# Optimization experiments

Measured on AMD Instinct MI355X. Metric: run time of the kernel, lower is better.

The kernel has to match this reference:

```python
import jax, jax.numpy as jnp
import numpy as np

BN_EPS = 1e-5

def _bn_train(x, g, b):
    # BatchNorm1d in training mode: biased batch stats over the row dim
    m = x.mean(0)
    v = x.var(0)
    return g * (x - m) * jax.lax.rsqrt(v + BN_EPS) + b


def setup_inputs() -> dict:
    key = jax.random.key(0)
    ks = jax.random.split(key, 16)
    N, V, C, H, T, NC, OD, EH, EC = 128, 128, 256, 512, 12, 5, 5, 256, 256
    s = 0.05
    idx = jax.random.randint(ks[1], (T, N), 0, NC)
    return {
        "x": jax.random.normal(ks[0], (N, V, C), jnp.float32),
        "hidden_states": jnp.zeros((N, V, H), jnp.float32),
        "cell_states": jnp.zeros((N, V, H), jnp.float32),
        "one_hots_c_pred_seq": jax.nn.one_hot(idx, NC, dtype=jnp.float32),
        "W_ih": jax.random.normal(ks[2], (4 * H, C), jnp.float32) * s,
        "W_hh": jax.random.normal(ks[3], (4 * H, H), jnp.float32) * s,
        "b_ih": jax.random.normal(ks[4], (4 * H,), jnp.float32) * s,
        "b_hh": jax.random.normal(ks[5], (4 * H,), jnp.float32) * s,
        "W_cls": jax.random.normal(ks[6], (NC, H), jnp.float32) * s,
        "b_cls": jax.random.normal(ks[7], (NC,), jnp.float32) * s,
        "W_eh": jax.random.normal(ks[8], (EH, H), jnp.float32) * s,
        "b_eh": jax.random.normal(ks[9], (EH,), jnp.float32) * s,
        "g_eh": jnp.ones((EH,), jnp.float32),
        "beta_eh": jnp.zeros((EH,), jnp.float32),
        "W_ec": jax.random.normal(ks[10], (EC, NC), jnp.float32) * s,
        "b_ec": jax.random.normal(ks[11], (EC,), jnp.float32) * s,
        "g_ec": jnp.ones((EC,), jnp.float32),
        "beta_ec": jnp.zeros((EC,), jnp.float32),
        "W_out": jax.random.normal(ks[12], (OD, EH + EC), jnp.float32) * s,
        "b_out": jax.random.normal(ks[13], (OD,), jnp.float32) * s,
    }


def reference(x, hidden_states, cell_states, one_hots_c_pred_seq,
              W_ih, W_hh, b_ih, b_hh, W_cls, b_cls,
              W_eh, b_eh, g_eh, beta_eh, W_ec, b_ec, g_ec, beta_ec,
              W_out, b_out):
    N, V, C = x.shape
    H = hidden_states.shape[-1]
    xf = x.reshape(N * V, C)
    gx = xf @ W_ih.T + b_ih  # input gates are identical every step (x is repeated)

    def step(carry, onehot):
        h, c = carry  # [N*V, H]
        gates = gx + h @ W_hh.T + b_hh
        i, f, g, o = jnp.split(gates, 4, axis=1)  # pytorch LSTMCell gate order
        c = jax.nn.sigmoid(f) * c + jax.nn.sigmoid(i) * jnp.tanh(g)
        h = jax.nn.sigmoid(o) * jnp.tanh(c)
        # ClassifierLayer: avg-pool over V then 1x1 conv == mean + linear
        oc = h.reshape(N, V, H).mean(1) @ W_cls.T + b_cls  # [N, nc]
        # PredictionLayer
        eh = jax.nn.relu(_bn_train(h @ W_eh.T + b_eh, g_eh, beta_eh))
        ohr = jnp.broadcast_to(onehot[:, None, :], (N, V, onehot.shape[-1])).reshape(N * V, -1)
        ec = jax.nn.relu(_bn_train(ohr @ W_ec.T + b_ec, g_ec, beta_ec))
        op = jnp.concatenate([eh, ec], axis=1) @ W_out.T + b_out  # [N*V, out_dim]
        return (h, c), (op.reshape(N, V, -1), oc)

    carry0 = (hidden_states.reshape(N * V, H), cell_states.reshape(N * V, H))
    _, (preds, c_outs) = jax.lax.scan(step, carry0, one_hots_c_pred_seq)
    preds = preds.transpose(1, 0, 2, 3)  # [N, T, V, out_dim]
    # output_activation: bivariate-Gaussian params
    pred_outs = jnp.stack([preds[..., 0], preds[..., 1],
                           jnp.exp(preds[..., 2]), jnp.exp(preds[..., 3]),
                           jnp.tanh(preds[..., 4])], axis=-1)
    return pred_outs, c_outs
```

## Files before the change

kernel.cpp:

```cpp
#include <hip/hip_runtime.h>
#include <hip/hip_bf16.h>
#include <stdint.h>

typedef __hip_bfloat16 bf16;
typedef __attribute__((ext_vector_type(8))) short bf16x8;
typedef __attribute__((ext_vector_type(4))) short bf16x4;
typedef __attribute__((ext_vector_type(4))) float f32x4;

#define NN 128
#define VV 128
#define CC 256
#define HH 512
#define TT 12
#define NCLS 5
#define OD 5
#define EHD 256
#define KCAT (HH + CC)
#define ROWS (NN * VV)
#define PRED_SZ (NN * TT * VV * OD)
#define LDP 72
#define MiB (1ull << 20)


__device__ __forceinline__ float sigm(float x) {
    return __builtin_amdgcn_rcpf(1.f + __expf(-x));
}
__device__ __forceinline__ float tanh_(float x) {
    x = fminf(fmaxf(x, -15.f), 15.f);
    float e = __expf(2.f * x);
    return (e - 1.f) * __builtin_amdgcn_rcpf(e + 1.f);
}
__device__ __forceinline__ float bf2f(unsigned short v) {
    unsigned u = ((unsigned)v) << 16; float f; __builtin_memcpy(&f, &u, 4); return f;
}
__device__ __forceinline__ float ldin(const void* p, int i, int is32) {
    return is32 ? ((const float*)p)[i] : __bfloat162float(((const bf16*)p)[i]);
}

__device__ __forceinline__ void gl_lds16(const bf16* g, bf16* l) {
    __builtin_amdgcn_global_load_lds(
        (const __attribute__((address_space(1))) unsigned int*)g,
        (__attribute__((address_space(3))) unsigned int*)l, 16, 0, 0);
}


__device__ __forceinline__ void stage_t128s(const bf16* __restrict__ g, int ldg, int row0, int k0,
                                            bf16* lds) {
    int lane = threadIdx.x & 63, wave = threadIdx.x >> 6;
#pragma unroll
    for (int j = 0; j < 2; ++j) {
        int slot = j * 256 + wave * 64 + lane;
        int lds_row = slot >> 3;
        int bx = ((slot & 7) * 16) ^ ((lds_row & 7) << 4);
        int r = lds_row + 64 * (bx >> 6);
        int cb = bx & 63;
        gl_lds16(g + (size_t)(row0 + r) * ldg + k0 + (cb >> 1), lds + slot * 8);
    }
}
__device__ __forceinline__ void stage_t64s(const bf16* __restrict__ g, int ldg, int row0, int k0,
                                           bf16* lds) {
    int lane = threadIdx.x & 63, wave = threadIdx.x >> 6;
    int slot = wave * 64 + lane;
    int lds_row = slot >> 3;
    int bx = ((slot & 7) * 16) ^ ((lds_row & 7) << 4);
    int r = lds_row + 32 * (bx >> 6);
    int cb = bx & 63;
    gl_lds16(g + (size_t)(row0 + r) * ldg + k0 + (cb >> 1), lds + slot * 8);
}
__device__ __forceinline__ bf16x8 swz_rd(const bf16* base, int lds_row, int half, int eb) {
    int off = lds_row * 128 + ((half * 64 + eb) ^ ((lds_row & 7) << 4));
    return *(const bf16x8*)((const char*)base + off);
}
__device__ __forceinline__ void mfma_step32(const bf16* As, const bf16* Bs, f32x4 acc[4][4]) {
    const int lane = threadIdx.x & 63, wave = threadIdx.x >> 6;
    const int ha = wave >> 1, hb = wave & 1;
    const int l15 = lane & 15, eb = (lane >> 4) * 16;
    bf16x8 af[4], bg[4];
#pragma unroll
    for (int x = 0; x < 4; ++x) {
        af[x] = swz_rd(As, x * 16 + l15, ha, eb);
        bg[x] = swz_rd(Bs, x * 16 + l15, hb, eb);
    }
#pragma unroll
    for (int bi = 0; bi < 4; ++bi)
#pragma unroll
        for (int bj = 0; bj < 4; ++bj)
            acc[bi][bj] = __builtin_amdgcn_mfma_f32_16x16x32_bf16(af[bi], bg[bj], acc[bi][bj], 0, 0, 0);
}

__device__ __forceinline__ void stage128(const bf16* __restrict__ A, int lda, int row0,
                                         const bf16* __restrict__ B, int ldb, int col0,
                                         int k, bf16* As, bf16* Bs) {
    int lane = threadIdx.x & 63, wave = threadIdx.x >> 6;
    const bf16* pA = A + (size_t)(row0 + wave * 32 + (lane >> 3)) * lda + k + (lane & 7) * 8;
    const bf16* pB = B + (size_t)(col0 + wave * 32 + (lane >> 3)) * ldb + k + (lane & 7) * 8;
    bf16* lA = As + wave * 2048 + lane * 8;
    bf16* lB = Bs + wave * 2048 + lane * 8;
#pragma unroll
    for (int j = 0; j < 4; ++j) {
        gl_lds16(pA + (size_t)(j * 8) * lda, lA + j * 512);
        gl_lds16(pB + (size_t)(j * 8) * ldb, lB + j * 512);
    }
}
__device__ __forceinline__ void tile_mfma64(const bf16* As, const bf16* Bs, f32x4 acc[4][4]) {
    const int lane = threadIdx.x & 63, wave = threadIdx.x >> 6;
    const int wro = (wave >> 1) * 64, wco = (wave & 1) * 64;
    const int l15 = lane & 15, l8 = (lane >> 4) * 8;
#pragma unroll
    for (int kk = 0; kk < 64; kk += 32) {
        bf16x8 af[4], bg[4];
#pragma unroll
        for (int x = 0; x < 4; ++x) {
            af[x] = *(const bf16x8*)(As + (wro + x * 16 + l15) * 64 + kk + l8);
            bg[x] = *(const bf16x8*)(Bs + (wco + x * 16 + l15) * 64 + kk + l8);
        }
#pragma unroll
        for (int bi = 0; bi < 4; ++bi)
#pragma unroll
            for (int bj = 0; bj < 4; ++bj)
                acc[bi][bj] = __builtin_amdgcn_mfma_f32_16x16x32_bf16(af[bi], bg[bj], acc[bi][bj], 0, 0, 0);
    }
}

__global__ void detect_dtype(const void* g_eh, int* flag, int* hnz) {
    unsigned w = *(const unsigned*)g_eh;
    *flag = (w == 0x3F800000u) ? 1 : 0;
    *hnz = 0;
}

__global__ __launch_bounds__(256) void convert_in(const void* src, bf16* dst, int n, const int* flag) {
    int is32 = *flag;
    int i = blockIdx.x * 256 + threadIdx.x;
    int stride = gridDim.x * 256;
    if (is32) { const float* s = (const float*)src; for (; i < n; i += stride) dst[i] = __float2bfloat16(s[i]); }
    else      { const bf16*  s = (const bf16*)src;  for (; i < n; i += stride) dst[i] = s[i]; }
}

__global__ __launch_bounds__(256) void convert_in_hflag(const void* src, bf16* dst, int n, const int* flag,
                                                        int* nz) {
    int is32 = *flag;
    int i = blockIdx.x * 256 + threadIdx.x;
    int stride = gridDim.x * 256;
    int loc = 0;
    if (is32) {
        const float* s = (const float*)src;
        for (; i < n; i += stride) { float v = s[i]; if (__float_as_uint(v) != 0u) loc = 1; dst[i] = __float2bfloat16(v); }
    } else {
        const bf16* s = (const bf16*)src;
        for (; i < n; i += stride) { bf16 v = s[i]; if (*(const unsigned short*)&v) loc = 1; dst[i] = v; }
    }
    if (loc) atomicOr(nz, 1);
}

__global__ __launch_bounds__(256) void init_c(const void* cell, bf16* c, const int* flag) {
    int is32 = *flag;
    size_t i = (size_t)blockIdx.x * 256 + threadIdx.x;
    const size_t total = (size_t)ROWS * HH;
    for (; i < total; i += (size_t)8192 * 256) c[i] = __float2bfloat16(ldin(cell, (int)i, is32));
}

__device__ __forceinline__ void issue_loads(const bf16* __restrict__ A, int lda, int row0, int ka,
                                            const bf16* __restrict__ B, int ldb, int col0, int kb,
                                            bf16x8 ar[4], bf16x8 br[4]) {
    int tid = threadIdx.x;
#pragma unroll
    for (int it = 0; it < 4; ++it) {
        int cidx = tid + 256 * it;
        int row = cidx >> 3;
        int cc8 = (cidx & 7) * 8;
        ar[it] = *(const bf16x8*)(A + (size_t)(row0 + row) * lda + ka + cc8);
        br[it] = *(const bf16x8*)(B + (size_t)(col0 + row) * ldb + kb + cc8);
    }
}
__device__ __forceinline__ void write_lds(bf16* As, bf16* Bs, const bf16x8 ar[4], const bf16x8 br[4]) {
    int tid = threadIdx.x;
#pragma unroll
    for (int it = 0; it < 4; ++it) {
        int cidx = tid + 256 * it;
        int row = cidx >> 3;
        int cc8 = (cidx & 7) * 8;
        *(bf16x8*)(As + row * LDP + cc8) = ar[it];
        *(bf16x8*)(Bs + row * LDP + cc8) = br[it];
    }
}
__device__ __forceinline__ void tile_mfma(const bf16* As, const bf16* Bs, f32x4 acc[4][4]) {
    const int lane = threadIdx.x & 63, wave = threadIdx.x >> 6;
    const int wro = (wave >> 1) * 64, wco = (wave & 1) * 64;
    const int l15 = lane & 15, l8 = (lane >> 4) * 8;
#pragma unroll
    for (int kk = 0; kk < 64; kk += 32) {
        bf16x8 af[4], bg[4];
#pragma unroll
        for (int x = 0; x < 4; ++x) {
            af[x] = *(const bf16x8*)(As + (wro + x * 16 + l15) * LDP + kk + l8);
            bg[x] = *(const bf16x8*)(Bs + (wco + x * 16 + l15) * LDP + kk + l8);
        }
#pragma unroll
        for (int bi = 0; bi < 4; ++bi)
#pragma unroll
            for (int bj = 0; bj < 4; ++bj)
                acc[bi][bj] = __builtin_amdgcn_mfma_f32_16x16x32_bf16(af[bi], bg[bj], acc[bi][bj], 0, 0, 0);
    }
}

__global__ __launch_bounds__(256) void prep_weights(const void* __restrict__ Wih, const void* __restrict__ Whh,
                                                    const void* __restrict__ bih, const void* __restrict__ bhh,
                                                    bf16* __restrict__ Wihp, bf16* __restrict__ Whhp,
                                                    float* __restrict__ biasp, const int* flag) {
    int is32 = *flag;
    int jg = blockIdx.x;
    int b = jg >> 7, j = jg & 127;
    int gate = (j >> 4) & 3;
    int unit = b * 32 + (j & 15) + 16 * (j >> 6);
    int p = gate * HH + unit;
    for (int k = threadIdx.x; k < HH; k += 256)
        Whhp[(size_t)jg * HH + k] = __float2bfloat16(ldin(Whh, p * HH + k, is32));
    for (int k = threadIdx.x; k < CC; k += 256)
        Wihp[(size_t)jg * CC + k] = __float2bfloat16(ldin(Wih, p * CC + k, is32));
    if (threadIdx.x == 0)
        biasp[jg] = ldin(bih, p, is32) + ldin(bhh, p, is32);
}

__global__ __launch_bounds__(256) void gemm_k0(const bf16* __restrict__ A, const bf16* __restrict__ B,
                                               const float* __restrict__ biasp, bf16* __restrict__ gx) {
    __shared__ bf16 As[128 * 64], Bs[128 * 64];
    f32x4 acc[4][4] = {};
    int row0 = blockIdx.x * 128, col0 = blockIdx.y * 128;
    for (int k0 = 0; k0 < CC; k0 += 64) {
        __syncthreads();
        stage128(A, CC, row0, B, CC, col0, k0, As, Bs);
        __syncthreads();
        tile_mfma64(As, Bs, acc);
    }
    int lane = threadIdx.x & 63, wave = threadIdx.x >> 6;
    int wro = (wave >> 1) * 64, wco = (wave & 1) * 64;
    int l15 = lane & 15, lr4 = (lane >> 4) * 4;
#pragma unroll
    for (int bj = 0; bj < 4; ++bj) {
        int j = wco + bj * 16 + l15;
        float bia = biasp[col0 + j];
        int sidx = wco + l15 * 4 + bj;
#pragma unroll
        for (int bi = 0; bi < 4; ++bi)
#pragma unroll
            for (int reg = 0; reg < 4; ++reg) {
                int r = row0 + wro + bi * 16 + lr4 + reg;
                gx[(size_t)r * 2048 + col0 + sidx] = __float2bfloat16(acc[bi][bj][reg] + bia);
            }
    }
}

__global__ __launch_bounds__(256) void ec_precompute(const void* __restrict__ W_ec, const void* __restrict__ b_ec,
                                                     const void* __restrict__ g_ec, const void* __restrict__ beta_ec,
                                                     const void* __restrict__ W_out, const void* __restrict__ b_out,
                                                     const void* __restrict__ onehot, float* __restrict__ ecd_all,
                                                     const int* flag) {
    __shared__ float ecv[NCLS][EHD];
    __shared__ float cntf[NCLS];
    __shared__ float ecdc[NCLS][OD];
    int is32 = *flag;
    int t = blockIdx.x, tid = threadIdx.x;
    int ohoff = t * NN * NCLS;
    if (tid < NCLS) {
        float cnum = 0.f;
        for (int n = 0; n < NN; ++n) cnum += ldin(onehot, ohoff + n * NCLS + tid, is32);
        cntf[tid] = cnum * (1.f / NN);
    }
    __syncthreads();
    {
        int j = tid;
        float vals[NCLS];
        float m = 0.f, e2 = 0.f;
        float be = ldin(b_ec, j, is32);
        for (int cc = 0; cc < NCLS; ++cc) {
            vals[cc] = ldin(W_ec, j * NCLS + cc, is32) + be;
            m += cntf[cc] * vals[cc];
            e2 += cntf[cc] * vals[cc] * vals[cc];
        }
        float rs = rsqrtf(e2 - m * m + 1e-5f);
        float g = ldin(g_ec, j, is32), bt = ldin(beta_ec, j, is32);
        for (int cc = 0; cc < NCLS; ++cc)
            ecv[cc][j] = fmaxf(g * (vals[cc] - m) * rs + bt, 0.f);
    }
    __syncthreads();
    if (tid < NCLS * OD) {
        int cc = tid / OD, k = tid % OD;
        float s = 0.f;
        for (int j = 0; j < EHD; ++j) s += ecv[cc][j] * ldin(W_out, k * (EHD * 2) + EHD + j, is32);
        ecdc[cc][k] = s;
    }
    __syncthreads();
    if (tid < NN) {
        for (int k = 0; k < OD; ++k) {
            float s = ldin(b_out, k, is32);
            for (int cc = 0; cc < NCLS; ++cc) s += ldin(onehot, ohoff + tid * NCLS + cc, is32) * ecdc[cc][k];
            ecd_all[((size_t)t * NN + tid) * OD + k] = s;
        }
    }
}

__device__ __forceinline__ void final_rows(int grp, const bf16* __restrict__ ehp, const float* __restrict__ colsum,
                                           const float* __restrict__ colss, const void* __restrict__ g_eh,
                                           const void* __restrict__ beta_eh, const float* __restrict__ ecd_all,
                                           const float* Wl, void* __restrict__ out, int t, int is32) {
    int wave = threadIdx.x >> 6, lane = threadIdx.x & 63;
    int r = grp * 4 + wave;
    int j0 = lane * 4;
    float av[4], bv[4];
#pragma unroll
    for (int e = 0; e < 4; ++e) {
        float mean = colsum[j0 + e] * (1.f / ROWS);
        float var = colss[j0 + e] * (1.f / ROWS) - mean * mean;
        float a = ldin(g_eh, j0 + e, is32) * rsqrtf(var + 1e-5f);
        av[e] = a;
        bv[e] = ldin(beta_eh, j0 + e, is32) - mean * a;
    }
    bf16x4 xs = *(const bf16x4*)(ehp + (size_t)r * EHD + j0);
    float v0 = fmaxf(av[0] * bf2f((unsigned short)xs[0]) + bv[0], 0.f);
    float v1 = fmaxf(av[1] * bf2f((unsigned short)xs[1]) + bv[1], 0.f);
    float v2 = fmaxf(av[2] * bf2f((unsigned short)xs[2]) + bv[2], 0.f);
    float v3 = fmaxf(av[3] * bf2f((unsigned short)xs[3]) + bv[3], 0.f);
    float p[OD];
#pragma unroll
    for (int k = 0; k < OD; ++k)
        p[k] = v0 * Wl[k * EHD + j0] + v1 * Wl[k * EHD + j0 + 1] + v2 * Wl[k * EHD + j0 + 2] + v3 * Wl[k * EHD + j0 + 3];
#pragma unroll
    for (int off = 32; off; off >>= 1)
#pragma unroll
        for (int k = 0; k < OD; ++k) p[k] += __shfl_down(p[k], off, 64);
    if (lane == 0) {
        int n = r >> 7, v = r & 127;
        const float* en = ecd_all + ((size_t)t * NN + n) * OD;
        float o0 = p[0] + en[0];
        float o1 = p[1] + en[1];
        float o2 = expf(p[2] + en[2]);
        float o3 = expf(p[3] + en[3]);
        float o4 = tanh_(p[4] + en[4]);
        size_t base = (size_t)n * (TT * VV * OD) + (size_t)t * (VV * OD) + (size_t)v * OD;
        if (is32) {
            float* dst = (float*)out + base;
            dst[0] = o0; dst[1] = o1; dst[2] = o2; dst[3] = o3; dst[4] = o4;
        } else {
            bf16* dst = (bf16*)out + base;
            dst[0] = __float2bfloat16(o0);
            dst[1] = __float2bfloat16(o1);
            dst[2] = __float2bfloat16(o2);
            dst[3] = __float2bfloat16(o3);
            dst[4] = __float2bfloat16(o4);
        }
    }
}

__global__ __launch_bounds__(256) void lstm_fused(const bf16* __restrict__ h_in, const bf16* __restrict__ Whhp,
                                                  const bf16* __restrict__ gx, bf16* __restrict__ c,
                                                  bf16* __restrict__ h_out, float* __restrict__ csum_cur,
                                                  float* __restrict__ colsum_z, float* __restrict__ colss_z,
                                                  const bf16* __restrict__ Weh, const void* __restrict__ b_eh,
                                                  bf16* __restrict__ ehp_w, float* __restrict__ colsum_w,
                                                  float* __restrict__ colss_w, const float* __restrict__ csum_prev,
                                                  const void* __restrict__ W_cls, const void* __restrict__ b_cls,
                                                  void* __restrict__ outp, int t_aux,
                                                  const bf16* __restrict__ ehp_r, const float* __restrict__ colsum_r,
                                                  const float* __restrict__ colss_r, const void* __restrict__ g_eh,
                                                  const void* __restrict__ beta_eh, const void* __restrict__ W_out,
                                                  const float* __restrict__ ecd_all, int t_final,
                                                  const int* __restrict__ flag) {
    __shared__ __align__(16) unsigned char smem[49152];
    int tid = threadIdx.x;
    if (blockIdx.x < 2048) {
        bf16* Asb[3] = { (bf16*)smem, (bf16*)(smem + 8192), (bf16*)(smem + 16384) };
        bf16* Bsb[3] = { (bf16*)(smem + 24576), (bf16*)(smem + 32768), (bf16*)(smem + 40960) };
        f32x4 acc[4][4] = {};
        bf16x4 gpre[16];
        unsigned short cpre[16];
        int row0 = (blockIdx.x & 127) * 128, col0 = (blockIdx.x >> 7) * 128;
        int lane = tid & 63, wave = tid >> 6;
        int wro = (wave >> 1) * 64;
        int l15 = lane & 15, lr4 = (lane >> 4) * 4;
        int ul = (wave & 1) * 16 + l15;
        int u = (blockIdx.x >> 7) * 32 + ul;
        const bf16* gxp = gx + col0 + (wave & 1) * 64 + l15 * 4;
        stage_t128s(h_in, HH, row0, 0, Asb[0]);
        stage_t128s(Whhp, HH, col0, 0, Bsb[0]);
        stage_t128s(h_in, HH, row0, 32, Asb[1]);
        stage_t128s(Whhp, HH, col0, 32, Bsb[1]);
#pragma unroll
        for (int s = 0; s < 16; ++s) {
            const bf16* Ac = Asb[s % 3];
            const bf16* Bc = Bsb[s % 3];
            if (s + 2 < 16) {
                stage_t128s(h_in, HH, row0, (s + 2) * 32, Asb[(s + 2) % 3]);
                stage_t128s(Whhp, HH, col0, (s + 2) * 32, Bsb[(s + 2) % 3]);
            }
            if (s == 0)       asm volatile("s_waitcnt vmcnt(8)" ::: "memory");
            else if (s < 14)  asm volatile("s_waitcnt vmcnt(10)" ::: "memory");
            else if (s == 14) asm volatile("s_waitcnt vmcnt(6)" ::: "memory");
            else              asm volatile("s_waitcnt vmcnt(2)" ::: "memory");
            __builtin_amdgcn_s_barrier();
            __builtin_amdgcn_sched_barrier(0);
            {
                int bi = s >> 2, reg = s & 3;
                int r = row0 + wro + bi * 16 + lr4 + reg;
                gpre[s] = *(const bf16x4*)(gxp + (size_t)r * 2048);
                cpre[s] = *(const unsigned short*)(c + (size_t)r * HH + u);
            }
            mfma_step32(Ac, Bc, acc);
            __builtin_amdgcn_sched_barrier(0);
            __builtin_amdgcn_s_barrier();
        }
        __syncthreads();
        float* hsum = (float*)smem;
        if (tid < 32) hsum[tid] = 0.f;
        if (blockIdx.x == 0) { colsum_z[tid] = 0.f; colss_z[tid] = 0.f; }
        __syncthreads();
        float hpart = 0.f;
#pragma unroll
        for (int bi = 0; bi < 4; ++bi) {
#pragma unroll
            for (int reg = 0; reg < 4; ++reg) {
                int idx = bi * 4 + reg;
                int r = row0 + wro + bi * 16 + lr4 + reg;
                float gi = acc[bi][0][reg] + bf2f((unsigned short)gpre[idx][0]);
                float gf = acc[bi][1][reg] + bf2f((unsigned short)gpre[idx][1]);
                float gg = acc[bi][2][reg] + bf2f((unsigned short)gpre[idx][2]);
                float go = acc[bi][3][reg] + bf2f((unsigned short)gpre[idx][3]);
                float iv = sigm(gi), fv = sigm(gf), gv = tanh_(gg), ov = sigm(go);
                size_t ci = (size_t)r * HH + u;
                float cn = fv * bf2f(cpre[idx]) + iv * gv;
                c[ci] = __float2bfloat16(cn);
                float hv = ov * tanh_(cn);
                h_out[ci] = __float2bfloat16(hv);
                hpart += hv;
            }
        }
        atomicAdd(&hsum[ul], hpart);
        __syncthreads();
        if (tid < 32) csum_cur[(size_t)(blockIdx.x & 127) * HH + (blockIdx.x >> 7) * 32 + tid] = hsum[tid];
        return;
    }
    int is32 = *flag;
    int b = blockIdx.x - 2048;
    if (b >= 640) {
        if (t_final < 0) return;
        float* Wl = (float*)smem;
        for (int i = tid; i < OD * EHD; i += 256)
            Wl[i] = ldin(W_out, (i >> 8) * (EHD * 2) + (i & 255), is32);
        __syncthreads();
        int fb = b - 640;
#pragma unroll
        for (int g = 0; g < 4; ++g)
            final_rows(fb * 4 + g, ehp_r, colsum_r, colss_r, g_eh, beta_eh, ecd_all, Wl, outp, t_final, is32);
        return;
    }
    if (b >= 512) {
        if (t_aux < 0) return;
        float* wl = (float*)smem;
        float* wred = (float*)(smem + 10240);
        int wave = tid >> 6, lane = tid & 63;
        for (int i = tid; i < NCLS * HH; i += 256) wl[i] = ldin(W_cls, i, is32);
        __syncthreads();
        int n = b - 512;
        float pk[NCLS] = {};
        for (int u = tid; u < HH; u += 256) {
            float cv = csum_prev[(size_t)n * HH + u];
#pragma unroll
            for (int k = 0; k < NCLS; ++k) pk[k] += cv * wl[k * HH + u];
        }
#pragma unroll
        for (int off = 32; off; off >>= 1)
#pragma unroll
            for (int k = 0; k < NCLS; ++k) pk[k] += __shfl_down(pk[k], off, 64);
        if (lane == 0)
#pragma unroll
            for (int k = 0; k < NCLS; ++k) wred[wave * NCLS + k] = pk[k];
        __syncthreads();
        if (tid < NCLS) {
            float a = (wred[tid] + wred[NCLS + tid] + wred[2 * NCLS + tid] + wred[3 * NCLS + tid]) * (1.f / VV)
                      + ldin(b_cls, tid, is32);
            int idx = PRED_SZ + t_aux * (NN * NCLS) + n * NCLS + tid;
            if (is32) ((float*)outp)[idx] = a;
            else      ((bf16*)outp)[idx] = __float2bfloat16(a);
        }
        return;
    }
    if (t_aux < 0) return;
    bf16* Asb[3] = { (bf16*)smem, (bf16*)(smem + 4096), (bf16*)(smem + 8192) };
    bf16* Bsb[3] = { (bf16*)(smem + 12288), (bf16*)(smem + 20480), (bf16*)(smem + 28672) };
    float* s_sum = (float*)(smem + 36864);
    float* s_ss  = (float*)(smem + 37376);
    f32x4 acc[4][2] = {};
    int row0 = (b >> 1) * 64, col0 = (b & 1) * 128;
    const int lane = tid & 63, wave = tid >> 6;
    const int l15 = lane & 15, eb = (lane >> 4) * 16;
    stage_t64s(h_in, HH, row0, 0, Asb[0]);
    stage_t128s(Weh, HH, col0, 0, Bsb[0]);
    stage_t64s(h_in, HH, row0, 32, Asb[1]);
    stage_t128s(Weh, HH, col0, 32, Bsb[1]);
#pragma unroll
    for (int s = 0; s < 16; ++s) {
        const bf16* Ac = Asb[s % 3];
        const bf16* Bc = Bsb[s % 3];
        if (s + 2 < 16) {
            stage_t64s(h_in, HH, row0, (s + 2) * 32, Asb[(s + 2) % 3]);
            stage_t128s(Weh, HH, col0, (s + 2) * 32, Bsb[(s + 2) % 3]);
        }
        if (s < 14)       asm volatile("s_waitcnt vmcnt(6)" ::: "memory");
        else if (s == 14) asm volatile("s_waitcnt vmcnt(3)" ::: "memory");
        else              asm volatile("s_waitcnt vmcnt(0)" ::: "memory");
        __builtin_amdgcn_s_barrier();
        __builtin_amdgcn_sched_barrier(0);
        bf16x8 af[4], bg[2];
#pragma unroll
        for (int x = 0; x < 4; ++x)
            af[x] = swz_rd(Ac, (x & 1) * 16 + l15, x >> 1, eb);
#pragma unroll
        for (int x = 0; x < 2; ++x)
            bg[x] = swz_rd(Bc, (wave & 1) * 32 + x * 16 + l15, wave >> 1, eb);
#pragma unroll
        for (int bi = 0; bi < 4; ++bi)
#pragma unroll
            for (int bj = 0; bj < 2; ++bj)
                acc[bi][bj] = __builtin_amdgcn_mfma_f32_16x16x32_bf16(af[bi], bg[bj], acc[bi][bj], 0, 0, 0);
        __builtin_amdgcn_sched_barrier(0);
        __builtin_amdgcn_s_barrier();
    }
    int lr4 = (lane >> 4) * 4;
    __syncthreads();
    if (tid < 128) { s_sum[tid] = 0.f; s_ss[tid] = 0.f; }
    __syncthreads();
#pragma unroll
    for (int bj = 0; bj < 2; ++bj) {
        int j = wave * 32 + bj * 16 + l15;
        int col = col0 + j;
        float bia = ldin(b_eh, col, is32);
        float ps = 0.f, pss = 0.f;
#pragma unroll
        for (int bi = 0; bi < 4; ++bi)
#pragma unroll
            for (int reg = 0; reg < 4; ++reg) {
                int r = row0 + bi * 16 + lr4 + reg;
                float val = acc[bi][bj][reg] + bia;
                ehp_w[(size_t)r * EHD + col] = __float2bfloat16(val);
                ps += val; pss += val * val;
            }
        atomicAdd(&s_sum[j], ps);
        atomicAdd(&s_ss[j], pss);
    }
    __syncthreads();
    if (tid < 128) {
        atomicAdd(&colsum_w[col0 + tid], s_sum[tid]);
        atomicAdd(&colss_w[col0 + tid], s_ss[tid]);
    }
}

__global__ __launch_bounds__(256) void lstm_gemm_gx_first(const bf16* __restrict__ h_in, const bf16* __restrict__ Whhp,
                                                          const bf16* __restrict__ gx, bf16* __restrict__ c,
                                                          bf16* __restrict__ h_out, float* __restrict__ csum,
                                                          float* __restrict__ colsum, float* __restrict__ colss,
                                                          const int* __restrict__ gemm_flag) {
    __shared__ bf16 As[128 * 64], Bs[128 * 64];
    __shared__ float hsum[32];
    f32x4 acc[4][4] = {};
    bf16x4 gpre[16];
    unsigned short cpre[16];
    int row0 = blockIdx.x * 128, col0 = blockIdx.y * 128;
    int tid = threadIdx.x, lane = tid & 63, wave = tid >> 6;
    int wro = (wave >> 1) * 64;
    int l15 = lane & 15, lr4 = (lane >> 4) * 4;
    int ul = (wave & 1) * 16 + l15;
    int u = blockIdx.y * 32 + ul;
    const bf16* gxp = gx + col0 + (wave & 1) * 64 + l15 * 4;
    const int do_gemm = *gemm_flag;
    if (do_gemm) {
#pragma unroll
        for (int k0 = 0; k0 < HH; k0 += 64) {
            __syncthreads();
            stage128(h_in, HH, row0, Whhp, HH, col0, k0, As, Bs);
            __syncthreads();
#pragma unroll
            for (int e = 0; e < 2; ++e) {
                int idx = (k0 >> 6) * 2 + e;
                int bi = idx >> 2, reg = idx & 3;
                int r = row0 + wro + bi * 16 + lr4 + reg;
                gpre[idx] = *(const bf16x4*)(gxp + (size_t)r * 2048);
                cpre[idx] = *(const unsigned short*)(c + (size_t)r * HH + u);
            }
            tile_mfma64(As, Bs, acc);
        }
    } else {
#pragma unroll
        for (int idx = 0; idx < 16; ++idx) {
            int bi = idx >> 2, reg = idx & 3;
            int r = row0 + wro + bi * 16 + lr4 + reg;
            gpre[idx] = *(const bf16x4*)(gxp + (size_t)r * 2048);
            cpre[idx] = *(const unsigned short*)(c + (size_t)r * HH + u);
        }
    }
    __syncthreads();
    if (tid < 32) hsum[tid] = 0.f;
    if (blockIdx.x == 0 && blockIdx.y == 0) { colsum[tid] = 0.f; colss[tid] = 0.f; }
    __syncthreads();
    float hpart = 0.f;
#pragma unroll
    for (int bi = 0; bi < 4; ++bi) {
#pragma unroll
        for (int reg = 0; reg < 4; ++reg) {
            int idx = bi * 4 + reg;
            int r = row0 + wro + bi * 16 + lr4 + reg;
            float gi = acc[bi][0][reg] + bf2f((unsigned short)gpre[idx][0]);
            float gf = acc[bi][1][reg] + bf2f((unsigned short)gpre[idx][1]);
            float gg = acc[bi][2][reg] + bf2f((unsigned short)gpre[idx][2]);
            float go = acc[bi][3][reg] + bf2f((unsigned short)gpre[idx][3]);
            float iv = sigm(gi), fv = sigm(gf), gv = tanh_(gg), ov = sigm(go);
            size_t ci = (size_t)r * HH + u;
            float cn = fv * bf2f(cpre[idx]) + iv * gv;
            c[ci] = __float2bfloat16(cn);
            float hv = ov * tanh_(cn);
            h_out[ci] = __float2bfloat16(hv);
            hpart += hv;
        }
    }
    atomicAdd(&hsum[ul], hpart);
    __syncthreads();
    if (tid < 32) csum[(size_t)blockIdx.x * HH + blockIdx.y * 32 + tid] = hsum[tid];
}

__global__ __launch_bounds__(256) void lstm_gemm_cat(const bf16* __restrict__ h_in, const bf16* __restrict__ x,
                                                     const bf16* __restrict__ Wihp, const bf16* __restrict__ Whhp,
                                                     const float* __restrict__ biasp, bf16* __restrict__ c,
                                                     bf16* __restrict__ h_out, float* __restrict__ csum,
                                                     float* __restrict__ colsum, float* __restrict__ colss) {
    __shared__ bf16 As[128 * LDP], Bs[128 * LDP];
    __shared__ float hsum[32];
    f32x4 acc[4][4] = {};
    bf16x8 ar[4], br[4];
    int row0 = blockIdx.x * 128, col0 = blockIdx.y * 128;
    issue_loads(h_in, HH, row0, 0, Whhp, HH, col0, 0, ar, br);
    for (int k0 = 0; k0 < KCAT; k0 += 64) {
        __syncthreads();
        write_lds(As, Bs, ar, br);
        __syncthreads();
        int kn = k0 + 64;
        if (kn < KCAT) {
            if (kn < HH) issue_loads(h_in, HH, row0, kn, Whhp, HH, col0, kn, ar, br);
            else         issue_loads(x, CC, row0, kn - HH, Wihp, CC, col0, kn - HH, ar, br);
        }
        tile_mfma(As, Bs, acc);
    }
    int tid = threadIdx.x;
    if (tid < 32) hsum[tid] = 0.f;
    if (blockIdx.x == 0 && blockIdx.y == 0) { colsum[tid] = 0.f; colss[tid] = 0.f; }
    __syncthreads();
    int lane = tid & 63, wave = tid >> 6;
    int wro = (wave >> 1) * 64;
    int l15 = lane & 15, lr4 = (lane >> 4) * 4;
    int ul = (wave & 1) * 16 + l15;
    int u = blockIdx.y * 32 + ul;
    int colp = col0 + (wave & 1) * 64 + l15;
    float b0 = biasp[colp], b1 = biasp[colp + 16], b2 = biasp[colp + 32], b3 = biasp[colp + 48];
    float hpart = 0.f;
#pragma unroll
    for (int bi = 0; bi < 4; ++bi) {
#pragma unroll
        for (int reg = 0; reg < 4; ++reg) {
            int r = row0 + wro + bi * 16 + lr4 + reg;
            float gi = acc[bi][0][reg] + b0;
            float gf = acc[bi][1][reg] + b1;
            float gg = acc[bi][2][reg] + b2;
            float go = acc[bi][3][reg] + b3;
            float iv = sigm(gi), fv = sigm(gf), gv = tanh_(gg), ov = sigm(go);
            size_t ci = (size_t)r * HH + u;
            float cn = fv * __bfloat162float(c[ci]) + iv * gv;
            c[ci] = __float2bfloat16(cn);
            float hv = ov * tanh_(cn);
            h_out[ci] = __float2bfloat16(hv);
            hpart += hv;
        }
    }
    atomicAdd(&hsum[ul], hpart);
    __syncthreads();
    if (tid < 32) csum[(size_t)blockIdx.x * HH + blockIdx.y * 32 + tid] = hsum[tid];
}

__global__ __launch_bounds__(256) void eh_cls(const bf16* __restrict__ A, const bf16* __restrict__ B,
                                              const void* __restrict__ bias, bf16* __restrict__ out,
                                              float* __restrict__ colsum, float* __restrict__ colss,
                                              const float* __restrict__ csum, const void* __restrict__ W_cls,
                                              const void* __restrict__ b_cls, void* __restrict__ outp,
                                              int t, const int* flag,
                                              const bf16* __restrict__ ehp_prev, const float* __restrict__ colsum_prev,
                                              const float* __restrict__ colss_prev, const void* __restrict__ g_eh,
                                              const void* __restrict__ beta_eh, const void* __restrict__ W_out,
                                              const float* __restrict__ ecd_all, int tprev) {
    __shared__ __align__(16) unsigned char smem[32768];
    int is32 = *flag;
    int tid = threadIdx.x;
    if (blockIdx.x >= 640) {
        if (tprev < 0) return;
        float* Wl = (float*)smem;
        for (int i = tid; i < OD * EHD; i += 256)
            Wl[i] = ldin(W_out, (i >> 8) * (EHD * 2) + (i & 255), is32);
        __syncthreads();
        int fb = blockIdx.x - 640;
#pragma unroll
        for (int g = 0; g < 4; ++g)
            final_rows(fb * 4 + g, ehp_prev, colsum_prev, colss_prev, g_eh, beta_eh,
                       ecd_all, Wl, outp, tprev, is32);
        return;
    }
    if (blockIdx.x >= 512) {
        float* wl = (float*)smem;
        float* wred = (float*)(smem + 10240);
        int wave = tid >> 6, lane = tid & 63;
        for (int i = tid; i < NCLS * HH; i += 256) wl[i] = ldin(W_cls, i, is32);
        __syncthreads();
        int n = blockIdx.x - 512;
        float pk[NCLS] = {};
        for (int u = tid; u < HH; u += 256) {
            float cv = csum[(size_t)n * HH + u];
#pragma unroll
            for (int k = 0; k < NCLS; ++k) pk[k] += cv * wl[k * HH + u];
        }
#pragma unroll
        for (int off = 32; off; off >>= 1)
#pragma unroll
            for (int k = 0; k < NCLS; ++k) pk[k] += __shfl_down(pk[k], off, 64);
        if (lane == 0)
#pragma unroll
            for (int k = 0; k < NCLS; ++k) wred[wave * NCLS + k] = pk[k];
        __syncthreads();
        if (tid < NCLS) {
            float a = (wred[tid] + wred[NCLS + tid] + wred[2 * NCLS + tid] + wred[3 * NCLS + tid]) * (1.f / VV)
                      + ldin(b_cls, tid, is32);
            int idx = PRED_SZ + t * (NN * NCLS) + n * NCLS + tid;
            if (is32) ((float*)outp)[idx] = a;
            else      ((bf16*)outp)[idx] = __float2bfloat16(a);
        }
        return;
    }
    bf16* As = (bf16*)smem;
    bf16* Bs = (bf16*)(smem + 8192);
    float* s_sum = (float*)(smem + 24576);
    float* s_ss  = (float*)(smem + 25088);
    f32x4 acc[4][2] = {};
    int row0 = (blockIdx.x >> 1) * 64, col0 = (blockIdx.x & 1) * 128;
    const int lane = tid & 63, wave = tid >> 6;
    const int l15 = lane & 15, l8 = (lane >> 4) * 8;
    const bf16* pA = A + (size_t)(row0 + wave * 16 + (lane >> 3)) * HH + (lane & 7) * 8;
    const bf16* pB = B + (size_t)(col0 + wave * 32 + (lane >> 3)) * HH + (lane & 7) * 8;
    bf16* lA = As + wave * 1024 + lane * 8;
    bf16* lB = Bs + wave * 2048 + lane * 8;
    for (int k0 = 0; k0 < HH; k0 += 64) {
        __syncthreads();
        gl_lds16(pA + k0, lA);
        gl_lds16(pA + 8 * HH + k0, lA + 512);
#pragma unroll
        for (int j = 0; j < 4; ++j) gl_lds16(pB + (size_t)(j * 8) * HH + k0, lB + j * 512);
        __syncthreads();
#pragma unroll
        for (int kk = 0; kk < 64; kk += 32) {
            bf16x8 af[4], bg[2];
#pragma unroll
            for (int x = 0; x < 4; ++x) af[x] = *(const bf16x8*)(As + (x * 16 + l15) * 64 + kk + l8);
#pragma unroll
            for (int x = 0; x < 2; ++x) bg[x] = *(const bf16x8*)(Bs + (wave * 32 + x * 16 + l15) * 64 + kk + l8);
#pragma unroll
            for (int bi = 0; bi < 4; ++bi)
#pragma unroll
                for (int bj = 0; bj < 2; ++bj)
                    acc[bi][bj] = __builtin_amdgcn_mfma_f32_16x16x32_bf16(af[bi], bg[bj], acc[bi][bj], 0, 0, 0);
        }
    }
    int lr4 = (lane >> 4) * 4;
    if (tid < 128) { s_sum[tid] = 0.f; s_ss[tid] = 0.f; }
    __syncthreads();
#pragma unroll
    for (int bj = 0; bj < 2; ++bj) {
        int j = wave * 32 + bj * 16 + l15;
        int col = col0 + j;
        float bia = ldin(bias, col, is32);
        float ps = 0.f, pss = 0.f;
#pragma unroll
        for (int bi = 0; bi < 4; ++bi)
#pragma unroll
            for (int reg = 0; reg < 4; ++reg) {
                int r = row0 + bi * 16 + lr4 + reg;
                float val = acc[bi][bj][reg] + bia;
                out[(size_t)r * EHD + col] = __float2bfloat16(val);
                ps += val; pss += val * val;
            }
        atomicAdd(&s_sum[j], ps);
        atomicAdd(&s_ss[j], pss);
    }
    __syncthreads();
    if (tid < 128) {
        atomicAdd(&colsum[col0 + tid], s_sum[tid]);
        atomicAdd(&colss[col0 + tid], s_ss[tid]);
    }
}

__global__ __launch_bounds__(256) void final_kernel(const bf16* __restrict__ eh_pre, const float* __restrict__ colsum,
                                                    const float* __restrict__ colss, const void* __restrict__ g_eh,
                                                    const void* __restrict__ beta_eh, const void* __restrict__ W_out,
                                                    const float* __restrict__ ecd_all, void* __restrict__ out,
                                                    int t, const int* flag) {
    __shared__ float Wl[OD * EHD];
    int is32 = *flag;
    for (int i = threadIdx.x; i < OD * EHD; i += 256)
        Wl[i] = ldin(W_out, (i >> 8) * (EHD * 2) + (i & 255), is32);
    __syncthreads();
    final_rows(blockIdx.x, eh_pre, colsum, colss, g_eh, beta_eh, ecd_all, Wl, out, t, is32);
}

extern "C" void kernel_launch(void* const* d_in, const int* in_sizes, int n_in,
                              void* d_out, int out_size, void* d_ws, size_t ws_size,
                              hipStream_t stream) {
    const void* x       = d_in[0];
    const void* hidden  = d_in[1];
    const void* cell    = d_in[2];
    const void* onehot  = d_in[3];
    const void* W_ih    = d_in[4];
    const void* W_hh    = d_in[5];
    const void* b_ih    = d_in[6];
    const void* b_hh    = d_in[7];
    const void* W_cls   = d_in[8];
    const void* b_cls   = d_in[9];
    const void* W_eh    = d_in[10];
    const void* b_eh    = d_in[11];
    const void* g_eh    = d_in[12];
    const void* beta_eh = d_in[13];
    const void* W_ec    = d_in[14];
    const void* b_ec    = d_in[15];
    const void* g_ec    = d_in[16];
    const void* beta_ec = d_in[17];
    const void* W_out   = d_in[18];
    const void* b_out   = d_in[19];

    const int use_gx = (ws_size >= 148 * MiB) ? 1 : 0;

    char* ws = (char*)d_ws;
    bf16*  cbuf = (bf16*)(ws);
    char*  tail = ws + 16 * MiB;
    bf16*  h0   = (bf16*)(ws + 32 * MiB);
    bf16*  h1   = (bf16*)(ws + 48 * MiB);
    bf16*  gxb  = (bf16*)(ws + 64 * MiB);
    bf16*  ehp0, *ehp1, *x_c, *Wihp, *Whhp, *Weh_c;
    if (use_gx) {
        ehp0  = (bf16*)(ws + 128 * MiB);
        x_c   = (bf16*)(ws + 136 * MiB);
        ehp1  = (bf16*)(ws + 136 * MiB);
        Wihp  = (bf16*)(ws + 144 * MiB);
        Whhp  = (bf16*)(ws + 145 * MiB);
        Weh_c = (bf16*)(ws + 147 * MiB);
    } else {
        ehp0  = (bf16*)(ws + 64 * MiB);
        x_c   = (bf16*)(ws + 72 * MiB);
        ehp1  = (bf16*)(ws + 80 * MiB);
        Wihp  = (bf16*)(ws + 88 * MiB);
        Whhp  = (bf16*)(ws + 89 * MiB);
        Weh_c = (bf16*)(ws + 91 * MiB);
    }
    float* biasp   = (float*)(tail);
    float* colsum3[3] = { (float*)(tail + 8192), (float*)(tail + 10240), (float*)(tail + 12288) };
    float* colss3[3]  = { (float*)(tail + 9216), (float*)(tail + 11264), (float*)(tail + 13312) };
    int*   dflag   = (int*)  (tail + 16384);
    int*   hnz     = (int*)  (tail + 16388);
    float* csum0   = (float*)(tail + 20480);
    float* csum1   = (float*)(tail + 20480 + 262144);
    float* ecd_all = (float*)(tail + 20480 + 524288);

    bf16*  ehp_b[2]  = { ehp0, ehp1 };
    float* csum_b[2] = { csum0, csum1 };

    detect_dtype<<<1, 1, 0, stream>>>(g_eh, dflag, hnz);
    convert_in<<<4096, 256, 0, stream>>>(x, x_c, ROWS * CC, dflag);
    convert_in_hflag<<<4096, 256, 0, stream>>>(hidden, h0, ROWS * HH, dflag, hnz);
    convert_in<<<512, 256, 0, stream>>>(W_eh, Weh_c, EHD * HH, dflag);
    init_c<<<8192, 256, 0, stream>>>(cell, cbuf, dflag);
    prep_weights<<<2048, 256, 0, stream>>>(W_ih, W_hh, b_ih, b_hh, Wihp, Whhp, biasp, dflag);
    ec_precompute<<<TT, 256, 0, stream>>>(W_ec, b_ec, g_ec, beta_ec, W_out, b_out, onehot, ecd_all, dflag);
    if (use_gx)
        gemm_k0<<<dim3(128, 16), 256, 0, stream>>>(x_c, Wihp, biasp, gxb);

    if (use_gx) {
        lstm_gemm_gx_first<<<dim3(128, 16), 256, 0, stream>>>(h0, Whhp, gxb, cbuf, h1, csum_b[0],
                                                              colsum3[0], colss3[0], hnz);
        for (int t = 1; t < TT; ++t) {
            const bf16* hin = (t & 1) ? h1 : h0;
            bf16* hout = (t & 1) ? h0 : h1;
            int tp = t - 1, tf = t - 2;
            lstm_fused<<<3712, 256, 0, stream>>>(
                hin, Whhp, gxb, cbuf, hout, csum_b[t & 1], colsum3[t % 3], colss3[t % 3],
                Weh_c, b_eh, ehp_b[tp & 1], colsum3[tp % 3], colss3[tp % 3], csum_b[tp & 1],
                W_cls, b_cls, d_out, tp,
                ehp_b[t & 1] , colsum3[(tf + 3) % 3], colss3[(tf + 3) % 3],
                g_eh, beta_eh, W_out, ecd_all, tf, dflag);
        }
        {
            int t = TT - 1;
            const bf16* h_last = (t & 1) ? h1 : h0;
            eh_cls<<<1664, 256, 0, stream>>>(h_last, Weh_c, b_eh, ehp_b[t & 1], colsum3[t % 3], colss3[t % 3],
                                             csum_b[t & 1], W_cls, b_cls, d_out, t, dflag,
                                             ehp_b[(t - 1) & 1], colsum3[(t - 1) % 3], colss3[(t - 1) % 3],
                                             g_eh, beta_eh, W_out, ecd_all, t - 1);
            final_kernel<<<4096, 256, 0, stream>>>(ehp_b[t & 1], colsum3[t % 3], colss3[t % 3],
                                                   g_eh, beta_eh, W_out, ecd_all, d_out, t, dflag);
        }
    } else {
        for (int t = 0; t < TT; ++t) {
            const bf16* hin = (t & 1) ? h1 : h0;
            bf16* hout = (t & 1) ? h0 : h1;
            lstm_gemm_cat<<<dim3(128, 16), 256, 0, stream>>>(hin, x_c, Wihp, Whhp, biasp, cbuf, hout,
                                                             csum_b[t & 1], colsum3[t % 3], colss3[t % 3]);
            eh_cls<<<1664, 256, 0, stream>>>(hout, Weh_c, b_eh, ehp_b[t & 1], colsum3[t % 3], colss3[t % 3],
                                             csum_b[t & 1], W_cls, b_cls, d_out, t, dflag,
                                             ehp_b[(t - 1) & 1], colsum3[((t - 1) + 3) % 3], colss3[((t - 1) + 3) % 3],
                                             g_eh, beta_eh, W_out, ecd_all, t - 1);
        }
        final_kernel<<<4096, 256, 0, stream>>>(ehp_b[(TT - 1) & 1], colsum3[(TT - 1) % 3], colss3[(TT - 1) % 3],
                                               g_eh, beta_eh, W_out, ecd_all, d_out, TT - 1, dflag);
    }
}
```

Before: 1.126 ms.

## Widen LSTM recurrent GEMM tiles to 128x256 and pipeline eh GEMM

The recurrent h@W_hh GEMM in the fused LSTM kernel now uses 128x256 tiles, so 1024 blocks replace 2048 and each wave holds a 4x8 accumulator. The gx and c prefetch during the k-loop is dropped in favour of loading them in the epilogue. LDS grows to 72KB and launch bounds request two blocks per CU. Separately, the eh_cls GEMM is changed from a synchronous 64-wide k loop to a triple-buffered swizzled pipeline like the LSTM one. The aim is more operand reuse and fewer stalls, at the cost of higher register and LDS pressure, which may lower occupancy.

New measurement: 1.096 ms. 2.7% less time.

```diff
diff --git a/kernel.cpp b/kernel.cpp
--- a/kernel.cpp
+++ b/kernel.cpp
@@ -70,22 +70,6 @@
 __device__ __forceinline__ bf16x8 swz_rd(const bf16* base, int lds_row, int half, int eb) {
     int off = lds_row * 128 + ((half * 64 + eb) ^ ((lds_row & 7) << 4));
     return *(const bf16x8*)((const char*)base + off);
-}
-__device__ __forceinline__ void mfma_step32(const bf16* As, const bf16* Bs, f32x4 acc[4][4]) {
-    const int lane = threadIdx.x & 63, wave = threadIdx.x >> 6;
-    const int ha = wave >> 1, hb = wave & 1;
-    const int l15 = lane & 15, eb = (lane >> 4) * 16;
-    bf16x8 af[4], bg[4];
-#pragma unroll
-    for (int x = 0; x < 4; ++x) {
-        af[x] = swz_rd(As, x * 16 + l15, ha, eb);
-        bg[x] = swz_rd(Bs, x * 16 + l15, hb, eb);
-    }
-#pragma unroll
-    for (int bi = 0; bi < 4; ++bi)
-#pragma unroll
-        for (int bj = 0; bj < 4; ++bj)
-            acc[bi][bj] = __builtin_amdgcn_mfma_f32_16x16x32_bf16(af[bi], bg[bj], acc[bi][bj], 0, 0, 0);
 }
 
 __device__ __forceinline__ void stage128(const bf16* __restrict__ A, int lda, int row0,
@@ -351,7 +335,7 @@
     }
 }
 
-__global__ __launch_bounds__(256) void lstm_fused(const bf16* __restrict__ h_in, const bf16* __restrict__ Whhp,
+__global__ __launch_bounds__(256, 2) void lstm_fused(const bf16* __restrict__ h_in, const bf16* __restrict__ Whhp,
                                                   const bf16* __restrict__ gx, bf16* __restrict__ c,
                                                   bf16* __restrict__ h_out, float* __restrict__ csum_cur,
                                                   float* __restrict__ colsum_z, float* __restrict__ colss_z,
@@ -365,81 +349,109 @@
                                                   const void* __restrict__ beta_eh, const void* __restrict__ W_out,
                                                   const float* __restrict__ ecd_all, int t_final,
                                                   const int* __restrict__ flag) {
-    __shared__ __align__(16) unsigned char smem[49152];
+    __shared__ __align__(16) unsigned char smem[73728];
     int tid = threadIdx.x;
-    if (blockIdx.x < 2048) {
+    if (blockIdx.x < 1024) {
         bf16* Asb[3] = { (bf16*)smem, (bf16*)(smem + 8192), (bf16*)(smem + 16384) };
-        bf16* Bsb[3] = { (bf16*)(smem + 24576), (bf16*)(smem + 32768), (bf16*)(smem + 40960) };
-        f32x4 acc[4][4] = {};
-        bf16x4 gpre[16];
-        unsigned short cpre[16];
-        int row0 = (blockIdx.x & 127) * 128, col0 = (blockIdx.x >> 7) * 128;
+        bf16* Bsb[3] = { (bf16*)(smem + 24576), (bf16*)(smem + 40960), (bf16*)(smem + 57344) };
+        f32x4 acc[4][8] = {};
+        int row0 = (blockIdx.x & 127) * 128;
+        int colb = blockIdx.x >> 7;
+        int col0 = colb * 256;
         int lane = tid & 63, wave = tid >> 6;
         int wro = (wave >> 1) * 64;
+        int ch  = wave & 1;
         int l15 = lane & 15, lr4 = (lane >> 4) * 4;
-        int ul = (wave & 1) * 16 + l15;
-        int u = (blockIdx.x >> 7) * 32 + ul;
-        const bf16* gxp = gx + col0 + (wave & 1) * 64 + l15 * 4;
+        int eb = (lane >> 4) * 16;
+        int cb = colb * 2 + ch;
         stage_t128s(h_in, HH, row0, 0, Asb[0]);
         stage_t128s(Whhp, HH, col0, 0, Bsb[0]);
+        stage_t128s(Whhp, HH, col0 + 128, 0, Bsb[0] + 4096);
         stage_t128s(h_in, HH, row0, 32, Asb[1]);
         stage_t128s(Whhp, HH, col0, 32, Bsb[1]);
+        stage_t128s(Whhp, HH, col0 + 128, 32, Bsb[1] + 4096);
 #pragma unroll
         for (int s = 0; s < 16; ++s) {
             const bf16* Ac = Asb[s % 3];
-            const bf16* Bc = Bsb[s % 3];
+            const bf16* Bc = Bsb[s % 3] + ch * 4096;
             if (s + 2 < 16) {
                 stage_t128s(h_in, HH, row0, (s + 2) * 32, Asb[(s + 2) % 3]);
                 stage_t128s(Whhp, HH, col0, (s + 2) * 32, Bsb[(s + 2) % 3]);
+                stage_t128s(Whhp, HH, col0 + 128, (s + 2) * 32, Bsb[(s + 2) % 3] + 4096);
             }
-            if (s == 0)       asm volatile("s_waitcnt vmcnt(8)" ::: "memory");
-            else if (s < 14)  asm volatile("s_waitcnt vmcnt(10)" ::: "memory");
+            if (s < 14)       asm volatile("s_waitcnt vmcnt(12)" ::: "memory");
             else if (s == 14) asm volatile("s_waitcnt vmcnt(6)" ::: "memory");
-            else              asm volatile("s_waitcnt vmcnt(2)" ::: "memory");
+            else              asm volatile("s_waitcnt vmcnt(0)" ::: "memory");
             __builtin_amdgcn_s_barrier();
             __builtin_amdgcn_sched_barrier(0);
-            {
-                int bi = s >> 2, reg = s & 3;
-                int r = row0 + wro + bi * 16 + lr4 + reg;
-                gpre[s] = *(const bf16x4*)(gxp + (size_t)r * 2048);
-                cpre[s] = *(const unsigned short*)(c + (size_t)r * HH + u);
-            }
-            mfma_step32(Ac, Bc, acc);
+            bf16x8 af[4], bg[8];
+#pragma unroll
+            for (int x = 0; x < 4; ++x)
+                af[x] = swz_rd(Ac, x * 16 + l15, wave >> 1, eb);
+#pragma unroll
+            for (int x = 0; x < 8; ++x)
+                bg[x] = swz_rd(Bc, (x & 3) * 16 + l15, x >> 2, eb);
+#pragma unroll
+            for (int bi = 0; bi < 4; ++bi)
+#pragma unroll
+                for (int bj = 0; bj < 8; ++bj)
+                    acc[bi][bj] = __builtin_amdgcn_mfma_f32_16x16x32_bf16(af[bi], bg[bj], acc[bi][bj], 0, 0, 0);
             __builtin_amdgcn_sched_barrier(0);
             __builtin_amdgcn_s_barrier();
         }
         __syncthreads();
         float* hsum = (float*)smem;
-        if (tid < 32) hsum[tid] = 0.f;
+        if (tid < 64) hsum[tid] = 0.f;
         if (blockIdx.x == 0) { colsum_z[tid] = 0.f; colss_z[tid] = 0.f; }
         __syncthreads();
-        float hpart = 0.f;
+        const bf16* gxp = gx + cb * 128 + l15 * 4;
+        int u0 = cb * 32 + l15, u1 = u0 + 16;
+        float hp0 = 0.f, hp1 = 0.f;
 #pragma unroll
         for (int bi = 0; bi < 4; ++bi) {
 #pragma unroll
             for (int reg = 0; reg < 4; ++reg) {
-                int idx = bi * 4 + reg;
                 int r = row0 + wro + bi * 16 + lr4 + reg;
-                float gi = acc[bi][0][reg] + bf2f((unsigned short)gpre[idx][0]);
-                float gf = acc[bi][1][reg] + bf2f((unsigned short)gpre[idx][1]);
-                float gg = acc[bi][2][reg] + bf2f((unsigned short)gpre[idx][2]);
-                float go = acc[bi][3][reg] + bf2f((unsigned short)gpre[idx][3]);
-                float iv = sigm(gi), fv = sigm(gf), gv = tanh_(gg), ov = sigm(go);
-                size_t ci = (size_t)r * HH + u;
-                float cn = fv * bf2f(cpre[idx]) + iv * gv;
-                c[ci] = __float2bfloat16(cn);
-                float hv = ov * tanh_(cn);
-                h_out[ci] = __float2bfloat16(hv);
-                hpart += hv;
+                bf16x4 g0 = *(const bf16x4*)(gxp + (size_t)r * 2048);
+                bf16x4 g1 = *(const bf16x4*)(gxp + (size_t)r * 2048 + 64);
+                unsigned short c0 = *(const unsigned short*)(c + (size_t)r * HH + u0);
+                unsigned short c1 = *(const unsigned short*)(c + (size_t)r * HH + u1);
+                {
+                    float gi = acc[bi][0][reg] + bf2f((unsigned short)g0[0]);
+                    float gf = acc[bi][1][reg] + bf2f((unsigned short)g0[1]);
+                    float gg = acc[bi][2][reg] + bf2f((unsigned short)g0[2]);
+                    float go = acc[bi][3][reg] + bf2f((unsigned short)g0[3]);
+                    float iv = sigm(gi), fv = sigm(gf), gv = tanh_(gg), ov = sigm(go);
+                    size_t ci = (size_t)r * HH + u0;
+                    float cn = fv * bf2f(c0) + iv * gv;
+                    c[ci] = __float2bfloat16(cn);
+                    float hv = ov * tanh_(cn);
+                    h_out[ci] = __float2bfloat16(hv);
+                    hp0 += hv;
+                }
+                {
+                    float gi = acc[bi][4][reg] + bf2f((unsigned short)g1[0]);
+                    float gf = acc[bi][5][reg] + bf2f((unsigned short)g1[1]);
+                    float gg = acc[bi][6][reg] + bf2f((unsigned short)g1[2]);
+                    float go = acc[bi][7][reg] + bf2f((unsigned short)g1[3]);
+                    float iv = sigm(gi), fv = sigm(gf), gv = tanh_(gg), ov = sigm(go);
+                    size_t ci = (size_t)r * HH + u1;
+                    float cn = fv * bf2f(c1) + iv * gv;
+                    c[ci] = __float2bfloat16(cn);
+                    float hv = ov * tanh_(cn);
+                    h_out[ci] = __float2bfloat16(hv);
+                    hp1 += hv;
+                }
             }
         }
-        atomicAdd(&hsum[ul], hpart);
-        __syncthreads();
-        if (tid < 32) csum_cur[(size_t)(blockIdx.x & 127) * HH + (blockIdx.x >> 7) * 32 + tid] = hsum[tid];
+        atomicAdd(&hsum[ch * 32 + l15], hp0);
+        atomicAdd(&hsum[ch * 32 + 16 + l15], hp1);
+        __syncthreads();
+        if (tid < 64) csum_cur[(size_t)(blockIdx.x & 127) * HH + colb * 64 + tid] = hsum[tid];
         return;
     }
     int is32 = *flag;
-    int b = blockIdx.x - 2048;
+    int b = blockIdx.x - 1024;
     if (b >= 640) {
         if (t_final < 0) return;
         float* Wl = (float*)smem;
@@ -692,7 +704,7 @@
                                               const float* __restrict__ colss_prev, const void* __restrict__ g_eh,
                                               const void* __restrict__ beta_eh, const void* __restrict__ W_out,
                                               const float* __restrict__ ecd_all, int tprev) {
-    __shared__ __align__(16) unsigned char smem[32768];
+    __shared__ __align__(16) unsigned char smem[38912];
     int is32 = *flag;
     int tid = threadIdx.x;
     if (blockIdx.x >= 640) {
@@ -738,40 +750,48 @@
         }
         return;
     }
-    bf16* As = (bf16*)smem;
-    bf16* Bs = (bf16*)(smem + 8192);
-    float* s_sum = (float*)(smem + 24576);
-    float* s_ss  = (float*)(smem + 25088);
+    bf16* Asb[3] = { (bf16*)smem, (bf16*)(smem + 4096), (bf16*)(smem + 8192) };
+    bf16* Bsb[3] = { (bf16*)(smem + 12288), (bf16*)(smem + 20480), (bf16*)(smem + 28672) };
+    float* s_sum = (float*)(smem + 36864);
+    float* s_ss  = (float*)(smem + 37376);
     f32x4 acc[4][2] = {};
     int row0 = (blockIdx.x >> 1) * 64, col0 = (blockIdx.x & 1) * 128;
     const int lane = tid & 63, wave = tid >> 6;
-    const int l15 = lane & 15, l8 = (lane >> 4) * 8;
-    const bf16* pA = A + (size_t)(row0 + wave * 16 + (lane >> 3)) * HH + (lane & 7) * 8;
-    const bf16* pB = B + (size_t)(col0 + wave * 32 + (lane >> 3)) * HH + (lane & 7) * 8;
-    bf16* lA = As + wave * 1024 + lane * 8;
-    bf16* lB = Bs + wave * 2048 + lane * 8;
-    for (int k0 = 0; k0 < HH; k0 += 64) {
-        __syncthreads();
-        gl_lds16(pA + k0, lA);
-        gl_lds16(pA + 8 * HH + k0, lA + 512);
-#pragma unroll
-        for (int j = 0; j < 4; ++j) gl_lds16(pB + (size_t)(j * 8) * HH + k0, lB + j * 512);
-        __syncthreads();
-#pragma unroll
-        for (int kk = 0; kk < 64; kk += 32) {
-            bf16x8 af[4], bg[2];
-#pragma unroll
-            for (int x = 0; x < 4; ++x) af[x] = *(const bf16x8*)(As + (x * 16 + l15) * 64 + kk + l8);
-#pragma unroll
-            for (int x = 0; x < 2; ++x) bg[x] = *(const bf16x8*)(Bs + (wave * 32 + x * 16 + l15) * 64 + kk + l8);
-#pragma unroll
-            for (int bi = 0; bi < 4; ++bi)
-#pragma unroll
-                for (int bj = 0; bj < 2; ++bj)
-                    acc[bi][bj] = __builtin_amdgcn_mfma_f32_16x16x32_bf16(af[bi], bg[bj], acc[bi][bj], 0, 0, 0);
-        }
+    const int l15 = lane & 15, eb = (lane >> 4) * 16;
+    stage_t64s(A, HH, row0, 0, Asb[0]);
+    stage_t128s(B, HH, col0, 0, Bsb[0]);
+    stage_t64s(A, HH, row0, 32, Asb[1]);
+    stage_t128s(B, HH, col0, 32, Bsb[1]);
+#pragma unroll
+    for (int s = 0; s < 16; ++s) {
+        const bf16* Ac = Asb[s % 3];
+        const bf16* Bc = Bsb[s % 3];
+        if (s + 2 < 16) {
+            stage_t64s(A, HH, row0, (s + 2) * 32, Asb[(s + 2) % 3]);
+            stage_t128s(B, HH, col0, (s + 2) * 32, Bsb[(s + 2) % 3]);
+        }
+        if (s < 14)       asm volatile("s_waitcnt vmcnt(6)" ::: "memory");
+        else if (s == 14) asm volatile("s_waitcnt vmcnt(3)" ::: "memory");
+        else              asm volatile("s_waitcnt vmcnt(0)" ::: "memory");
+        __builtin_amdgcn_s_barrier();
+        __builtin_amdgcn_sched_barrier(0);
+        bf16x8 af[4], bg[2];
+#pragma unroll
+        for (int x = 0; x < 4; ++x)
+            af[x] = swz_rd(Ac, (x & 1) * 16 + l15, x >> 1, eb);
+#pragma unroll
+        for (int x = 0; x < 2; ++x)
+            bg[x] = swz_rd(Bc, (wave & 1) * 32 + x * 16 + l15, wave >> 1, eb);
+#pragma unroll
+        for (int bi = 0; bi < 4; ++bi)
+#pragma unroll
+            for (int bj = 0; bj < 2; ++bj)
+                acc[bi][bj] = __builtin_amdgcn_mfma_f32_16x16x32_bf16(af[bi], bg[bj], acc[bi][bj], 0, 0, 0);
+        __builtin_amdgcn_sched_barrier(0);
+        __builtin_amdgcn_s_barrier();
     }
     int lr4 = (lane >> 4) * 4;
+    __syncthreads();
     if (tid < 128) { s_sum[tid] = 0.f; s_ss[tid] = 0.f; }
     __syncthreads();
 #pragma unroll
@@ -889,7 +909,7 @@
             const bf16* hin = (t & 1) ? h1 : h0;
             bf16* hout = (t & 1) ? h0 : h1;
             int tp = t - 1, tf = t - 2;
-            lstm_fused<<<3712, 256, 0, stream>>>(
+            lstm_fused<<<2688, 256, 0, stream>>>(
                 hin, Whhp, gxb, cbuf, hout, csum_b[t & 1], colsum3[t % 3], colss3[t % 3],
                 Weh_c, b_eh, ehp_b[tp & 1], colsum3[tp % 3], colss3[tp % 3], csum_b[tp & 1],
                 W_cls, b_cls, d_out, tp,
```
